# Kernel tuning notes

Hardware: AMD Instinct MI355X
Metric: run time of the kernel (lower is better)

Reference implementation:

```python
import jax, jax.numpy as jnp
import numpy as np


def P1(X):
    # Projection onto {X : X @ 1 = 1, 1^T X = 1} under Frobenius norm.
    # Expanding the original matrix expression:
    #   P1(X)[i,j] = X[i,j] + 1/n + sum(X)/n^2 - row_sum[i]/n - col_sum[j]/n
    n = X.shape[1]
    row = X.sum(axis=1, keepdims=True)          # [n,1]
    col = X.sum(axis=0, keepdims=True)          # [1,n]
    s = row.sum()                               # scalar total
    return X + (1.0 / n + s / (n * n)) - row / n - col / n


def setup_inputs() -> dict:
    key = jax.random.key(0)
    n = 4096
    X = jax.random.normal(key, (n, n), dtype=jnp.float32)
    return {"X": X, "max_iters": 20}


def reference(X, max_iters):
    # Dykstra-style alternating projection: X <- P1(X); early-return if
    # min(X) >= 0, else X <- relu(X); up to max_iters iterations.
    # Fixed-length scan with a `done` flag reproduces the data-dependent
    # early exit while staying jit-compatible.
    def step(carry, _):
        Xc, done = carry
        Xp = P1(Xc)
        nonneg = jnp.min(Xp) >= 0
        # If converged this iter: return the un-relu'd projection; else relu.
        Xn = jnp.where(nonneg, Xp, jax.nn.relu(Xp))
        Xout = jnp.where(done, Xc, Xn)
        return (Xout, done | nonneg), None

    (Xf, _), _ = jax.lax.scan(step, (X, jnp.array(False)), None, length=max_iters)
    return Xf
```

## Files before the change

kernel.cpp:

```cpp
#include <hip/hip_runtime.h>


#define NN    4096
#define NV4   1024
#define RPB   16
#define NBLK  256
#define ITERS 20
#define INV_N (1.0f / 4096.0f)
#define PSTR  21

typedef unsigned long long u64;
typedef float f32x4 __attribute__((ext_vector_type(4)));

__device__ __forceinline__ float wave_reduce_sum(float v) {
    #pragma unroll
    for (int m = 1; m < 64; m <<= 1) v += __shfl_xor(v, m, 64);
    return v;
}

__device__ __forceinline__ void st_atomic_f32x2(float* p, float a, float b) {
    u64 u = (u64)__float_as_uint(a) | ((u64)__float_as_uint(b) << 32);
    __hip_atomic_store((u64*)p, u, __ATOMIC_RELAXED, __HIP_MEMORY_SCOPE_AGENT);
}
__device__ __forceinline__ float2 ld_atomic_f32x2(const float* p) {
    u64 u = __hip_atomic_load((const u64*)p, __ATOMIC_RELAXED,
                              __HIP_MEMORY_SCOPE_AGENT);
    return make_float2(__uint_as_float((unsigned)u),
                       __uint_as_float((unsigned)(u >> 32)));
}

__device__ __forceinline__ void wait_flags(const u64* flags, int wave, int lane, u64 tgt) {
    if (lane < 16) {
        const u64* f = flags + (size_t)(wave * 16 + lane) * 8;
        while (__hip_atomic_load(f, __ATOMIC_RELAXED, __HIP_MEMORY_SCOPE_AGENT) < tgt)
            __builtin_amdgcn_s_sleep(1);
    }
    asm volatile("" ::: "memory");
}

__global__ __launch_bounds__(1024, 4)
void persist8(const float* __restrict__ X0, float* __restrict__ Xout,
              float* __restrict__ colpart,
              float* __restrict__ col_out,
              u64* __restrict__ flag1,
              u64* __restrict__ flag2)
{
    const int t    = threadIdx.x;
    const int wave = t >> 6;
    const int lane = t & 63;
    const int b    = blockIdx.x;
    const int row0 = b * RPB;

    __shared__ float part[1024 * PSTR];
    __shared__ f32x4 wql[64];
    __shared__ float rowsum[RPB];
    __shared__ float sred[16];

    f32x4 x[RPB];
    const f32x4* x0 = (const f32x4*)X0;
    #pragma unroll
    for (int r = 0; r < RPB; ++r)
        x[r] = x0[(size_t)(row0 + r) * NV4 + t];

    for (unsigned iter = 0; iter < ITERS; ++iter) {
        const u64 tgt = (u64)iter + 1;

        f32x4 cacc = x[0];
        #pragma unroll
        for (int r = 1; r < RPB; ++r) cacc += x[r];
        {
            float* cp = colpart + (size_t)b * NN + 4 * t;
            st_atomic_f32x2(cp,     cacc.x, cacc.y);
            st_atomic_f32x2(cp + 2, cacc.z, cacc.w);
        }
        #pragma unroll
        for (int r = 0; r < RPB; ++r)
            part[t * PSTR + r] = (x[r].x + x[r].y) + (x[r].z + x[r].w);
        asm volatile("s_waitcnt vmcnt(0)" ::: "memory");
        __syncthreads();
        if (t == 0)
            __hip_atomic_store(flag1 + (size_t)b * 8, tgt,
                               __ATOMIC_RELAXED, __HIP_MEMORY_SCOPE_AGENT);
        {
            float v = 0.f;
            #pragma unroll
            for (int k = 0; k < 16; ++k)
                v += part[(lane + 64 * k) * PSTR + wave];
            v = wave_reduce_sum(v);
            if (lane == 0) rowsum[wave] = v;
        }

        wait_flags(flag1, wave, lane, tgt);
        {
            const int blk = 16 * wave + (lane >> 2);
            const int q   = lane & 3;
            const float* cp = colpart + (size_t)blk * NN + (b << 4) + 4 * q;
            float2 a01 = ld_atomic_f32x2(cp);
            float2 a23 = ld_atomic_f32x2(cp + 2);
            f32x4 v; v.x = a01.x; v.y = a01.y; v.z = a23.x; v.w = a23.y;
            #pragma unroll
            for (int m = 4; m <= 32; m <<= 1) {
                v.x += __shfl_xor(v.x, m, 64);
                v.y += __shfl_xor(v.y, m, 64);
                v.z += __shfl_xor(v.z, m, 64);
                v.w += __shfl_xor(v.w, m, 64);
            }
            if (lane < 4) wql[wave * 4 + lane] = v;
        }
        __syncthreads();
        if (wave == 0) {
            f32x4 u = wql[lane];
            #pragma unroll
            for (int m = 4; m <= 32; m <<= 1) {
                u.x += __shfl_xor(u.x, m, 64);
                u.y += __shfl_xor(u.y, m, 64);
                u.z += __shfl_xor(u.z, m, 64);
                u.w += __shfl_xor(u.w, m, 64);
            }
            if (lane < 4) {
                float* co = col_out + (b << 4) + 4 * lane;
                st_atomic_f32x2(co,     u.x, u.y);
                st_atomic_f32x2(co + 2, u.z, u.w);
            }
            asm volatile("s_waitcnt vmcnt(0)" ::: "memory");
        }
        __syncthreads();
        if (t == 0)
            __hip_atomic_store(flag2 + (size_t)b * 8, tgt,
                               __ATOMIC_RELAXED, __HIP_MEMORY_SCOPE_AGENT);

        wait_flags(flag2, wave, lane, tgt);
        float2 ab = ld_atomic_f32x2(col_out + 4 * t);
        float2 cd = ld_atomic_f32x2(col_out + 4 * t + 2);
        f32x4 cv; cv.x = ab.x; cv.y = ab.y; cv.z = cd.x; cv.w = cd.y;
        {
            float cs = (cv.x + cv.y) + (cv.z + cv.w);
            cs = wave_reduce_sum(cs);
            if (lane == 0) sred[wave] = cs;
        }
        __syncthreads();
        float s = 0.f;
        #pragma unroll
        for (int w = 0; w < 16; ++w) s += sred[w];

        const float c0 = INV_N + s * (INV_N * INV_N);
        const f32x4 csub = cv * INV_N;
        #pragma unroll
        for (int r = 0; r < RPB; ++r) {
            const float a = c0 - rowsum[r] * INV_N;
            x[r].x = fmaxf(x[r].x + a - csub.x, 0.f);
            x[r].y = fmaxf(x[r].y + a - csub.y, 0.f);
            x[r].z = fmaxf(x[r].z + a - csub.z, 0.f);
            x[r].w = fmaxf(x[r].w + a - csub.w, 0.f);
        }
    }

    f32x4* xo = (f32x4*)Xout;
    #pragma unroll
    for (int r = 0; r < RPB; ++r)
        xo[(size_t)(row0 + r) * NV4 + t] = x[r];
}

extern "C" void kernel_launch(void* const* d_in, const int* in_sizes, int n_in,
                              void* d_out, int out_size, void* d_ws, size_t ws_size,
                              hipStream_t stream)
{
    const float* X0 = (const float*)d_in[0];
    float* X = (float*)d_out;

    float* colpart = (float*)d_ws;
    float* col_out = colpart + (size_t)NBLK * NN;
    u64*   flag1   = (u64*)(col_out + NN);
    u64*   flag2   = flag1 + NBLK * 8;

    hipMemsetAsync((void*)flag1, 0, 2 * NBLK * 8 * sizeof(u64), stream);

    persist8<<<dim3(NBLK), dim3(1024), 0, stream>>>(X0, X, colpart, col_out,
                                                    flag1, flag2);
}
```

Before: 266.5 us.

## Switch to 2D tile decomposition with single-phase flag exchange and double-buffered partials

Each block now owns a 256x256 tile (16x16 grid of blocks) instead of 16 full rows. It publishes column and row partial sums plus a block total with one tagged flag per iteration. Each block waits only on the blocks in its tile row and column (plus all totals), which replaces the previous two global barrier phases with one. Partial buffers alternate between two parity slots, guarded by a per-row-group read counter, so the next iteration's writes cannot overwrite data still being read. This trades more complex cross-block synchronization and polling of 256 totals per block for less global serialization.

```diff
diff --git a/kernel.cpp b/kernel.cpp
--- a/kernel.cpp
+++ b/kernel.cpp
@@ -3,11 +3,9 @@
 
 #define NN    4096
 #define NV4   1024
-#define RPB   16
 #define NBLK  256
 #define ITERS 20
 #define INV_N (1.0f / 4096.0f)
-#define PSTR  21
 
 typedef unsigned long long u64;
 typedef float f32x4 __attribute__((ext_vector_type(4)));
@@ -17,137 +15,159 @@
     for (int m = 1; m < 64; m <<= 1) v += __shfl_xor(v, m, 64);
     return v;
 }
-
-__device__ __forceinline__ void st_atomic_f32x2(float* p, float a, float b) {
-    u64 u = (u64)__float_as_uint(a) | ((u64)__float_as_uint(b) << 32);
-    __hip_atomic_store((u64*)p, u, __ATOMIC_RELAXED, __HIP_MEMORY_SCOPE_AGENT);
-}
-__device__ __forceinline__ float2 ld_atomic_f32x2(const float* p) {
-    u64 u = __hip_atomic_load((const u64*)p, __ATOMIC_RELAXED,
-                              __HIP_MEMORY_SCOPE_AGENT);
-    return make_float2(__uint_as_float((unsigned)u),
-                       __uint_as_float((unsigned)(u >> 32)));
-}
-
-__device__ __forceinline__ void wait_flags(const u64* flags, int wave, int lane, u64 tgt) {
-    if (lane < 16) {
-        const u64* f = flags + (size_t)(wave * 16 + lane) * 8;
-        while (__hip_atomic_load(f, __ATOMIC_RELAXED, __HIP_MEMORY_SCOPE_AGENT) < tgt)
-            __builtin_amdgcn_s_sleep(1);
-    }
-    asm volatile("" ::: "memory");
-}
+__device__ __forceinline__ void st_b64(u64* p, u64 v) {
+    __hip_atomic_store(p, v, __ATOMIC_RELAXED, __HIP_MEMORY_SCOPE_AGENT);
+}
+__device__ __forceinline__ u64 ld_b64(const u64* p) {
+    return __hip_atomic_load(p, __ATOMIC_RELAXED, __HIP_MEMORY_SCOPE_AGENT);
+}
+__device__ __forceinline__ u64 packf2(float a, float b) {
+    return (u64)__float_as_uint(a) | ((u64)__float_as_uint(b) << 32);
+}
+__device__ __forceinline__ float lo32(u64 u) { return __uint_as_float((unsigned)u); }
+__device__ __forceinline__ float hi32(u64 u) { return __uint_as_float((unsigned)(u >> 32)); }
 
 __global__ __launch_bounds__(1024, 4)
-void persist8(const float* __restrict__ X0, float* __restrict__ Xout,
-              float* __restrict__ colpart,
-              float* __restrict__ col_out,
-              u64* __restrict__ flag1,
-              u64* __restrict__ flag2)
+void persist9(const float* __restrict__ X0, float* __restrict__ Xout,
+              u64* __restrict__ colF,
+              u64* __restrict__ rowF,
+              u64* __restrict__ pflag,
+              u64* __restrict__ rdg)
 {
     const int t    = threadIdx.x;
-    const int wave = t >> 6;
     const int lane = t & 63;
+    const int g    = t >> 6;
+    const int c    = lane;
     const int b    = blockIdx.x;
-    const int row0 = b * RPB;
-
-    __shared__ float part[1024 * PSTR];
-    __shared__ f32x4 wql[64];
-    __shared__ float rowsum[RPB];
-    __shared__ float sred[16];
-
-    f32x4 x[RPB];
-    const f32x4* x0 = (const f32x4*)X0;
-    #pragma unroll
-    for (int r = 0; r < RPB; ++r)
-        x[r] = x0[(size_t)(row0 + r) * NV4 + t];
-
-    for (unsigned iter = 0; iter < ITERS; ++iter) {
-        const u64 tgt = (u64)iter + 1;
+    const int bi   = b >> 4;
+    const int bj   = b & 15;
+
+    __shared__ float part[16][64][17];
+    __shared__ f32x4 cq[16][64];
+    __shared__ f32x4 rq4[16][64];
+    __shared__ float bsv[256];
+    __shared__ f32x4 colq[64];
+    __shared__ float rsum[256];
+    __shared__ float sG;
+
+    f32x4 x[16];
+    {
+        const f32x4* xi = (const f32x4*)X0;
+        const size_t base = (size_t)(bi * 256 + g * 16) * NV4 + (bj * 64 + c);
+        #pragma unroll
+        for (int r = 0; r < 16; ++r)
+            x[r] = xi[base + (size_t)r * NV4];
+    }
+
+    for (int iter = 0; iter < ITERS; ++iter) {
+        const int p = iter & 1;
+        const u64 tagv = (u64)(iter + 1);
+
+        if (iter >= 2) {
+            if (lane < 16) {
+                const u64 need = (u64)16 * (u64)(iter >> 1);
+                const u64* f = rdg + (p * 16 + lane);
+                while (ld_b64(f) < need) __builtin_amdgcn_s_sleep(1);
+            }
+            asm volatile("" ::: "memory");
+        }
 
         f32x4 cacc = x[0];
         #pragma unroll
-        for (int r = 1; r < RPB; ++r) cacc += x[r];
+        for (int r = 1; r < 16; ++r) cacc += x[r];
+        cq[g][c] = cacc;
+        #pragma unroll
+        for (int r = 0; r < 16; ++r)
+            part[g][c][r] = (x[r].x + x[r].y) + (x[r].z + x[r].w);
+        __syncthreads();
+
+        float bs = 0.f;
+        if (g == 0) {
+            f32x4 v = cq[0][c];
+            #pragma unroll
+            for (int k = 1; k < 16; ++k) v += cq[k][c];
+            u64* dst = colF + (((size_t)(p * NBLK + b)) << 7) + 2 * c;
+            st_b64(dst,     packf2(v.x, v.y));
+            st_b64(dst + 1, packf2(v.z, v.w));
+            bs = wave_reduce_sum((v.x + v.y) + (v.z + v.w));
+        }
         {
-            float* cp = colpart + (size_t)b * NN + 4 * t;
-            st_atomic_f32x2(cp,     cacc.x, cacc.y);
-            st_atomic_f32x2(cp + 2, cacc.z, cacc.w);
-        }
-        #pragma unroll
-        for (int r = 0; r < RPB; ++r)
-            part[t * PSTR + r] = (x[r].x + x[r].y) + (x[r].z + x[r].w);
+            const int r = lane & 15, q = lane >> 4;
+            float v = 0.f;
+            #pragma unroll
+            for (int k = 0; k < 16; ++k) v += part[g][q * 16 + k][r];
+            v += __shfl_xor(v, 16, 64);
+            v += __shfl_xor(v, 32, 64);
+            float vp = __shfl_xor(v, 1, 64);
+            if (lane < 16 && (lane & 1) == 0) {
+                u64* dst = rowF + (((size_t)(p * NBLK + b)) << 7) + 8 * g + (lane >> 1);
+                st_b64(dst, packf2(v, vp));
+            }
+        }
         asm volatile("s_waitcnt vmcnt(0)" ::: "memory");
         __syncthreads();
         if (t == 0)
-            __hip_atomic_store(flag1 + (size_t)b * 8, tgt,
-                               __ATOMIC_RELAXED, __HIP_MEMORY_SCOPE_AGENT);
+            st_b64(pflag + (p * NBLK + b),
+                   (tagv << 32) | (u64)__float_as_uint(bs));
+
+        const int fcsrc = g * 16 + bj;
+        const int frsrc = bi * 16 + g;
         {
+            const u64* fc = pflag + (p * NBLK + fcsrc);
+            const u64* fr = pflag + (p * NBLK + frsrc);
+            const u64* fb = pflag + (p * NBLK + (t & 255));
+            bool dc = false, dr = false, db = (t >= 256);
+            u64 ub = 0;
+            while (true) {
+                if (!dc && (ld_b64(fc) >> 32) == tagv) dc = true;
+                if (!dr && (ld_b64(fr) >> 32) == tagv) dr = true;
+                if (!db) { u64 u = ld_b64(fb);
+                           if ((u >> 32) == tagv) { ub = u; db = true; } }
+                if (dc && dr && db) break;
+                __builtin_amdgcn_s_sleep(1);
+            }
+            if (t < 256) bsv[t] = lo32(ub);
+        }
+        asm volatile("" ::: "memory");
+        {
+            const u64* cp = colF + (((size_t)(p * NBLK + fcsrc)) << 7) + 2 * c;
+            const u64* rp = rowF + (((size_t)(p * NBLK + frsrc)) << 7) + 2 * c;
+            u64 c0 = ld_b64(cp), c1 = ld_b64(cp + 1);
+            u64 r0 = ld_b64(rp), r1 = ld_b64(rp + 1);
+            f32x4 cv, rv;
+            cv.x = lo32(c0); cv.y = hi32(c0); cv.z = lo32(c1); cv.w = hi32(c1);
+            rv.x = lo32(r0); rv.y = hi32(r0); rv.z = lo32(r1); rv.w = hi32(r1);
+            cq[g][c]  = cv;
+            rq4[g][c] = rv;
+        }
+        __syncthreads();
+        if (t == 0)
+            __hip_atomic_fetch_add(rdg + (p * 16 + bi), (u64)1,
+                                   __ATOMIC_RELAXED, __HIP_MEMORY_SCOPE_AGENT);
+        if (g == 0) {
+            f32x4 v = cq[0][c];
+            #pragma unroll
+            for (int k = 1; k < 16; ++k) v += cq[k][c];
+            colq[c] = v;
+        } else if (g >= 4 && g < 8) {
+            const int row = t - 256;
+            const float* rqf = (const float*)rq4;
             float v = 0.f;
             #pragma unroll
-            for (int k = 0; k < 16; ++k)
-                v += part[(lane + 64 * k) * PSTR + wave];
+            for (int k = 0; k < 16; ++k) v += rqf[k * 256 + row];
+            rsum[row] = v;
+        } else if (g == 8) {
+            float v = bsv[lane] + bsv[64 + lane] + bsv[128 + lane] + bsv[192 + lane];
             v = wave_reduce_sum(v);
-            if (lane == 0) rowsum[wave] = v;
-        }
-
-        wait_flags(flag1, wave, lane, tgt);
-        {
-            const int blk = 16 * wave + (lane >> 2);
-            const int q   = lane & 3;
-            const float* cp = colpart + (size_t)blk * NN + (b << 4) + 4 * q;
-            float2 a01 = ld_atomic_f32x2(cp);
-            float2 a23 = ld_atomic_f32x2(cp + 2);
-            f32x4 v; v.x = a01.x; v.y = a01.y; v.z = a23.x; v.w = a23.y;
-            #pragma unroll
-            for (int m = 4; m <= 32; m <<= 1) {
-                v.x += __shfl_xor(v.x, m, 64);
-                v.y += __shfl_xor(v.y, m, 64);
-                v.z += __shfl_xor(v.z, m, 64);
-                v.w += __shfl_xor(v.w, m, 64);
-            }
-            if (lane < 4) wql[wave * 4 + lane] = v;
-        }
-        __syncthreads();
-        if (wave == 0) {
-            f32x4 u = wql[lane];
-            #pragma unroll
-            for (int m = 4; m <= 32; m <<= 1) {
-                u.x += __shfl_xor(u.x, m, 64);
-                u.y += __shfl_xor(u.y, m, 64);
-                u.z += __shfl_xor(u.z, m, 64);
-                u.w += __shfl_xor(u.w, m, 64);
-            }
-            if (lane < 4) {
-                float* co = col_out + (b << 4) + 4 * lane;
-                st_atomic_f32x2(co,     u.x, u.y);
-                st_atomic_f32x2(co + 2, u.z, u.w);
-            }
-            asm volatile("s_waitcnt vmcnt(0)" ::: "memory");
-        }
-        __syncthreads();
-        if (t == 0)
-            __hip_atomic_store(flag2 + (size_t)b * 8, tgt,
-                               __ATOMIC_RELAXED, __HIP_MEMORY_SCOPE_AGENT);
-
-        wait_flags(flag2, wave, lane, tgt);
-        float2 ab = ld_atomic_f32x2(col_out + 4 * t);
-        float2 cd = ld_atomic_f32x2(col_out + 4 * t + 2);
-        f32x4 cv; cv.x = ab.x; cv.y = ab.y; cv.z = cd.x; cv.w = cd.y;
-        {
-            float cs = (cv.x + cv.y) + (cv.z + cv.w);
-            cs = wave_reduce_sum(cs);
-            if (lane == 0) sred[wave] = cs;
-        }
-        __syncthreads();
-        float s = 0.f;
-        #pragma unroll
-        for (int w = 0; w < 16; ++w) s += sred[w];
-
-        const float c0 = INV_N + s * (INV_N * INV_N);
-        const f32x4 csub = cv * INV_N;
-        #pragma unroll
-        for (int r = 0; r < RPB; ++r) {
-            const float a = c0 - rowsum[r] * INV_N;
+            if (lane == 0) sG = v;
+        }
+        __syncthreads();
+
+        const float cc0 = INV_N + sG * (INV_N * INV_N);
+        const f32x4 csub = colq[c] * INV_N;
+        #pragma unroll
+        for (int r = 0; r < 16; ++r) {
+            const float a = cc0 - rsum[g * 16 + r] * INV_N;
             x[r].x = fmaxf(x[r].x + a - csub.x, 0.f);
             x[r].y = fmaxf(x[r].y + a - csub.y, 0.f);
             x[r].z = fmaxf(x[r].z + a - csub.z, 0.f);
@@ -155,10 +175,13 @@
         }
     }
 
-    f32x4* xo = (f32x4*)Xout;
-    #pragma unroll
-    for (int r = 0; r < RPB; ++r)
-        xo[(size_t)(row0 + r) * NV4 + t] = x[r];
+    {
+        f32x4* xo = (f32x4*)Xout;
+        const size_t base = (size_t)(bi * 256 + g * 16) * NV4 + (bj * 64 + c);
+        #pragma unroll
+        for (int r = 0; r < 16; ++r)
+            xo[base + (size_t)r * NV4] = x[r];
+    }
 }
 
 extern "C" void kernel_launch(void* const* d_in, const int* in_sizes, int n_in,
@@ -168,13 +191,13 @@
     const float* X0 = (const float*)d_in[0];
     float* X = (float*)d_out;
 
-    float* colpart = (float*)d_ws;
-    float* col_out = colpart + (size_t)NBLK * NN;
-    u64*   flag1   = (u64*)(col_out + NN);
-    u64*   flag2   = flag1 + NBLK * 8;
-
-    hipMemsetAsync((void*)flag1, 0, 2 * NBLK * 8 * sizeof(u64), stream);
-
-    persist8<<<dim3(NBLK), dim3(1024), 0, stream>>>(X0, X, colpart, col_out,
-                                                    flag1, flag2);
-}
+    u64* colF  = (u64*)d_ws;
+    u64* rowF  = colF + 2 * NBLK * 128;
+    u64* pflag = rowF + 2 * NBLK * 128;
+    u64* rdg   = pflag + 2 * NBLK;
+
+    hipMemsetAsync((void*)pflag, 0, (2 * NBLK + 2 * 16) * sizeof(u64), stream);
+
+    persist9<<<dim3(NBLK), dim3(1024), 0, stream>>>(X0, X, colF, rowF,
+                                                    pflag, rdg);
+}
```

After: 270.5 us. No clear change (+1.5%).
